# Performance work log

Hardware: AMD Instinct MI355X
Metric: run time of the kernel (lower is better)

Reference implementation:

```python
import jax, jax.numpy as jnp
import numpy as np

HIDDEN_DIM = 4096
NUM_EXPERTS = 64
THRESHOLD = 0.8


def setup_inputs() -> dict:
    key = jax.random.key(0)
    kx, kw = jax.random.split(key)
    x = jax.random.normal(kx, (4, 4096, HIDDEN_DIM), dtype=jnp.float32)
    # gate weight init: normal(0, 0.1), bias zeros (as in nn.init calls)
    W = jax.random.normal(kw, (HIDDEN_DIM, NUM_EXPERTS), dtype=jnp.float32) * 0.1
    b = jnp.zeros((NUM_EXPERTS,), dtype=jnp.float32)
    return {"x": x, "W": W, "b": b}


def reference(x, W, b):
    # logits: [B, S, E]
    logits = jnp.einsum('bsh,he->bse', x, W) + b
    probs = jax.nn.softmax(logits, axis=-1)
    # descending sort over experts
    order = jnp.argsort(-probs, axis=-1)                        # [B,S,E] int
    sorted_probs = jnp.take_along_axis(probs, order, axis=-1)   # [B,S,E]
    cum = jnp.cumsum(sorted_probs, axis=-1)
    mask = cum >= THRESHOLD                                     # [B,S,E] bool
    k_values = jnp.argmax(mask.astype(jnp.float32), axis=-1) + 1
    never = ~jnp.any(mask, axis=-1)
    k_values = jnp.where(never, NUM_EXPERTS, k_values)          # [B,S] int
    # Vectorized mask-and-scatter replacing the per-token Python loop.
    # Padded to NUM_EXPERTS (static max_k) for jit compatibility; slots
    # beyond k get expert=-1, prob=0 exactly as the torch fill defaults.
    slot = jnp.arange(NUM_EXPERTS)                              # [E]
    sel = slot[None, None, :] < k_values[..., None]             # [B,S,E]
    selected_experts = jnp.where(sel, order, -1)
    selected_probs = jnp.where(sel, sorted_probs, 0.0)
    return selected_experts, selected_probs, k_values
```

## Files before the change

kernel.cpp:

```cpp
#include <hip/hip_runtime.h>
#include <math.h>

#define HID 4096
#define NEXP 64
#define NTOK 16384
#define NCH 16

typedef __attribute__((ext_vector_type(8))) short short8;
typedef __attribute__((ext_vector_type(8))) __bf16 bf16x8;
typedef __attribute__((ext_vector_type(4))) float f32x4;

__global__ __launch_bounds__(256) void wfrag_kernel(
    const float* __restrict__ W, short* __restrict__ wfh,
    short* __restrict__ wfl, unsigned int* __restrict__ flag_count) {
  if (blockIdx.x == 0 && threadIdx.x == 0) *flag_count = 0u;
  int gid = blockIdx.x * 256 + threadIdx.x;
  int l  = gid & 63;
  int nt = (gid >> 6) & 3;
  int ks = gid >> 8;
  int e  = nt * 16 + (l & 15);
  int k0 = ks * 32 + (l >> 4) * 8;
  bf16x8 h8, l8;
#pragma unroll
  for (int j = 0; j < 8; ++j) {
    float w = W[(size_t)(k0 + j) * NEXP + e];
    __bf16 h = (__bf16)w;
    h8[j] = h;
    l8[j] = (__bf16)(w - (float)h);
  }
  ((short8*)wfh)[gid] = __builtin_bit_cast(short8, h8);
  ((short8*)wfl)[gid] = __builtin_bit_cast(short8, l8);
}

template <int P>
__device__ __forceinline__ void issue_b(const short8*& wh, const short8*& wl,
                                        short8 (&rbh)[2][8],
                                        short8 (&rbl)[2][8]) {
#pragma unroll
  for (int kk = 0; kk < 2; ++kk)
#pragma unroll
    for (int nt = 0; nt < 4; ++nt) {
      rbh[P][kk * 4 + nt] = wh[kk * 256 + nt * 64];
      rbl[P][kk * 4 + nt] = wl[kk * 256 + nt * 64];
    }
  wh += 512;
  wl += 512;
}

template <int P>
__device__ __forceinline__ void issue_g(const float* (&xp)[4][2],
                                        float* stage ) {
#pragma unroll
  for (int st = 0; st < 4; ++st)
#pragma unroll
    for (int n = 0; n < 4; ++n)
      __builtin_amdgcn_global_load_lds(xp[st][n & 1] + (n >> 1) * (8 * HID),
                                       stage + st * 1024 + n * 256, 16, 0, 0);
#pragma unroll
  for (int st = 0; st < 4; ++st) {
    xp[st][0] += 64;
    xp[st][1] += 64;
  }
}

template <int P>
__device__ __forceinline__ void compute_c(const float* stage,
                                          short8 (&rbh)[2][8],
                                          short8 (&rbl)[2][8],
                                          f32x4 (&acc)[4][4], int l) {
  const int lr = l >> 4;
  const char* cb = (const char*)stage;
#pragma unroll
  for (int kk = 0; kk < 2; ++kk) {
    int s0 = ((kk * 8 + lr * 2) ^ (l & 7)) * 16;
#pragma unroll
    for (int st = 0; st < 4; ++st) {
      const char* rowbase = cb + st * 4096 + (l & 15) * 256;
      float4 lo = *(const float4*)(rowbase + s0);
      float4 hi = *(const float4*)(rowbase + (s0 ^ 16));
      float xv[8] = {lo.x, lo.y, lo.z, lo.w, hi.x, hi.y, hi.z, hi.w};
      bf16x8 ah, al;
#pragma unroll
      for (int j = 0; j < 8; ++j) {
        __bf16 h = (__bf16)xv[j];
        ah[j] = h;
        al[j] = (__bf16)(xv[j] - (float)h);
      }
#pragma unroll
      for (int nt = 0; nt < 4; ++nt) {
        bf16x8 vh = __builtin_bit_cast(bf16x8, rbh[P][kk * 4 + nt]);
        bf16x8 vl = __builtin_bit_cast(bf16x8, rbl[P][kk * 4 + nt]);
        acc[st][nt] = __builtin_amdgcn_mfma_f32_16x16x32_bf16(ah, vh, acc[st][nt], 0, 0, 0);
        acc[st][nt] = __builtin_amdgcn_mfma_f32_16x16x32_bf16(al, vh, acc[st][nt], 0, 0, 0);
        acc[st][nt] = __builtin_amdgcn_mfma_f32_16x16x32_bf16(ah, vl, acc[st][nt], 0, 0, 0);
        acc[st][nt] = __builtin_amdgcn_mfma_f32_16x16x32_bf16(al, vl, acc[st][nt], 0, 0, 0);
      }
    }
  }
}

#define SB __builtin_amdgcn_sched_barrier(0)
#define WAIT32 asm volatile("s_waitcnt vmcnt(32)" ::: "memory")
#define WAIT0  asm volatile("s_waitcnt vmcnt(0)" ::: "memory")

__global__ __launch_bounds__(256) void gemm_kernel(
    const float* __restrict__ x, const short* __restrict__ wfh,
    const short* __restrict__ wfl, float* __restrict__ partial) {
  __shared__ float xstage[4][2][4096];

  const int t = threadIdx.x;
  const int q = t >> 6;
  const int l = t & 63;
  const int lr = l >> 4;
  const int m0 = blockIdx.x * 64;
  const int kq = q * (HID / 4);

  const float* xp[4][2];
#pragma unroll
  for (int st = 0; st < 4; ++st)
#pragma unroll
    for (int p = 0; p < 2; ++p) {
      int g = (l & 15) ^ (lr + 4 * p);
      int row = m0 + st * 16 + 4 * p + lr;
      xp[st][p] = x + (size_t)row * HID + kq + g * 4;
    }

  const short8* wh = (const short8*)wfh + (size_t)(q * 32) * 256 + l;
  const short8* wl = (const short8*)wfl + (size_t)(q * 32) * 256 + l;

  f32x4 acc[4][4];
#pragma unroll
  for (int st = 0; st < 4; ++st)
#pragma unroll
    for (int nt = 0; nt < 4; ++nt) acc[st][nt] = (f32x4){0.f, 0.f, 0.f, 0.f};

  short8 rbh[2][8], rbl[2][8];

  issue_b<0>(wh, wl, rbh, rbl);
  SB;
  issue_g<0>(xp, &xstage[q][0][0]);
  SB;

#pragma unroll 1
  for (int c2 = 0; c2 < 7; ++c2) {
    issue_b<1>(wh, wl, rbh, rbl);
    SB;
    issue_g<1>(xp, &xstage[q][1][0]);
    SB;
    WAIT32;
    SB;
    compute_c<0>(&xstage[q][0][0], rbh, rbl, acc, l);

    issue_b<0>(wh, wl, rbh, rbl);
    SB;
    issue_g<0>(xp, &xstage[q][0][0]);
    SB;
    WAIT32;
    SB;
    compute_c<1>(&xstage[q][1][0], rbh, rbl, acc, l);
  }
  issue_b<1>(wh, wl, rbh, rbl);
  SB;
  issue_g<1>(xp, &xstage[q][1][0]);
  SB;
  WAIT32;
  SB;
  compute_c<0>(&xstage[q][0][0], rbh, rbl, acc, l);
  WAIT0;
  SB;
  compute_c<1>(&xstage[q][1][0], rbh, rbl, acc, l);

#pragma unroll
  for (int st = 0; st < 4; ++st)
#pragma unroll
    for (int nt = 0; nt < 4; ++nt)
#pragma unroll
      for (int r = 0; r < 4; ++r)
        partial[((size_t)q * NTOK + m0 + st * 16 + lr * 4 + r) * NEXP +
                nt * 16 + (l & 15)] = acc[st][nt][r];
}

__global__ __launch_bounds__(256) void route_kernel(
    const float* __restrict__ partial, const float* __restrict__ b,
    float* __restrict__ out_exp, float* __restrict__ out_prob,
    float* __restrict__ out_k, unsigned int* __restrict__ flag_count,
    int* __restrict__ flag_list) {
  const int tok = (int)((blockIdx.x * 256 + threadIdx.x) >> 6);
  const int l   = threadIdx.x & 63;

  float p0 = partial[((size_t)0 * NTOK + tok) * NEXP + l];
  float p1 = partial[((size_t)1 * NTOK + tok) * NEXP + l];
  float p2 = partial[((size_t)2 * NTOK + tok) * NEXP + l];
  float p3 = partial[((size_t)3 * NTOK + tok) * NEXP + l];
  float lgv = (p0 + p1) + (p2 + p3) + b[l];

  float mx = lgv;
#pragma unroll
  for (int off = 32; off; off >>= 1) mx = fmaxf(mx, __shfl_xor(mx, off));
  float ev = expf(lgv - mx);
  float sm = ev;
#pragma unroll
  for (int off = 32; off; off >>= 1) sm += __shfl_xor(sm, off);
  float p = ev / sm;

  float sp = p;
  int   si = l;
#pragma unroll
  for (int k = 2; k <= 64; k <<= 1) {
#pragma unroll
    for (int j = k >> 1; j > 0; j >>= 1) {
      float op = __shfl_xor(sp, j);
      int   oi = __shfl_xor(si, j);
      bool cmp  = (sp > op) || (sp == op && si < oi);
      bool keep = (cmp == (((l & k) == 0) == ((l & j) == 0)));
      if (!keep) { sp = op; si = oi; }
    }
  }

  float c = sp;
#pragma unroll
  for (int off = 1; off < 64; off <<= 1) {
    float tp = __shfl_up(c, off);
    if (l >= off) c += tp;
  }

  unsigned long long m = __ballot(c >= 0.8f);
  int kv = (m == 0ULL) ? NEXP : __ffsll(m);

  float spn = __shfl_down(sp, 1);
  bool pairRisk = (l < kv) && (l < 63) && ((sp - spn) < 1e-3f * (sp + spn));
  bool cumRisk  = fabsf(c - 0.8f) < 3e-4f;
  bool flagged  = (__ballot(pairRisk || cumRisk) != 0ULL);

  bool sel = l < kv;
  size_t base = (size_t)tok * NEXP;
  out_exp[base + l]  = sel ? (float)si : -1.0f;
  out_prob[base + l] = sel ? sp : 0.0f;
  if (l == 0) {
    out_k[tok] = (float)kv;
    if (flagged) {
      unsigned int idx = atomicAdd(flag_count, 1u);
      flag_list[idx] = tok;
    }
  }
}

__global__ __launch_bounds__(256) void router_repair(
    const float* __restrict__ x, const float* __restrict__ W,
    const float* __restrict__ b, const unsigned int* __restrict__ flag_count,
    const int* __restrict__ flag_list, float* __restrict__ out_exp,
    float* __restrict__ out_prob, float* __restrict__ out_k) {
  __shared__ double part[4][NEXP];
  const int t = threadIdx.x;
  const int e = t & 63;
  const int c = t >> 6;
  const int n = (int)*flag_count;

  for (int i = blockIdx.x; i < n; i += gridDim.x) {
    const int tok = flag_list[i];
    const float* xrow = x + (size_t)tok * HID;
    double s = 0.0;
    const int k0 = c * (HID / 4);
#pragma unroll 8
    for (int k = k0; k < k0 + HID / 4; ++k)
      s = fma((double)xrow[k], (double)W[(size_t)k * NEXP + e], s);
    part[c][e] = s;
    __syncthreads();

    if (t < 64) {
      double lgv = ((part[0][e] + part[1][e]) + part[2][e]) + part[3][e] +
                   (double)b[e];
      double mx = lgv;
#pragma unroll
      for (int off = 32; off; off >>= 1) mx = fmax(mx, __shfl_xor(mx, off));
      double ev = exp(lgv - mx);
      double sm = ev;
#pragma unroll
      for (int off = 32; off; off >>= 1) sm += __shfl_xor(sm, off);
      double p = ev / sm;

      double sp = p;
      int    si = e;
#pragma unroll
      for (int k = 2; k <= 64; k <<= 1) {
#pragma unroll
        for (int j = k >> 1; j > 0; j >>= 1) {
          double op = __shfl_xor(sp, j);
          int    oi = __shfl_xor(si, j);
          bool cmp  = (sp > op) || (sp == op && si < oi);
          bool keep = (cmp == (((e & k) == 0) == ((e & j) == 0)));
          if (!keep) { sp = op; si = oi; }
        }
      }

      double cc = sp;
#pragma unroll
      for (int off = 1; off < 64; off <<= 1) {
        double tp = __shfl_up(cc, off);
        if (e >= off) cc += tp;
      }

      unsigned long long m = __ballot(cc >= 0.8);
      int kv = (m == 0ULL) ? NEXP : __ffsll(m);

      bool sel = e < kv;
      size_t base = (size_t)tok * NEXP;
      out_exp[base + e]  = sel ? (float)si : -1.0f;
      out_prob[base + e] = sel ? (float)sp : 0.0f;
      if (e == 0) out_k[tok] = (float)kv;
    }
    __syncthreads();
  }
}

extern "C" void kernel_launch(void* const* d_in, const int* in_sizes, int n_in,
                              void* d_out, int out_size, void* d_ws,
                              size_t ws_size, hipStream_t stream) {
  const float* x = (const float*)d_in[0];
  const float* W = (const float*)d_in[1];
  const float* b = (const float*)d_in[2];

  float* out_exp  = (float*)d_out;
  float* out_prob = out_exp + (size_t)NTOK * NEXP;
  float* out_k    = out_prob + (size_t)NTOK * NEXP;

  short* wfh = (short*)d_ws;
  short* wfl = (short*)((char*)d_ws + (size_t)512 * 1024);
  unsigned int* flag_count = (unsigned int*)((char*)d_ws + (size_t)1024 * 1024);
  int* flag_list = (int*)((char*)d_ws + (size_t)1024 * 1024 + 256);
  float* partial = (float*)((char*)d_ws + (size_t)2 * 1024 * 1024);

  wfrag_kernel<<<128, 256, 0, stream>>>(W, wfh, wfl, flag_count);
  gemm_kernel<<<NTOK / 64, 256, 0, stream>>>(x, wfh, wfl, partial);
  route_kernel<<<NTOK * NEXP / 256, 256, 0, stream>>>(
      partial, b, out_exp, out_prob, out_k, flag_count, flag_list);
  router_repair<<<128, 256, 0, stream>>>(x, W, b, flag_count, flag_list,
                                         out_exp, out_prob, out_k);
}
```

Baseline: 125.3 us.

## Fuse routing epilogue into GEMM kernel via shared-memory partial reduction

The routing softmax, sort, cumulative threshold and output writes are folded into the GEMM kernel. The four per-wave K-split partial accumulators go to padded shared memory (reusing the x staging buffer) instead of a global partial buffer. Each wave then reduces them and routes 16 tokens. This removes a kernel launch and the global write and re-read of the partial logits. In exchange the GEMM blocks run a serial per-token routing tail that may not overlap well with other blocks' memory traffic.

```diff
diff --git a/kernel.cpp b/kernel.cpp
--- a/kernel.cpp
+++ b/kernel.cpp
@@ -4,7 +4,7 @@
 #define HID 4096
 #define NEXP 64
 #define NTOK 16384
-#define NCH 16
+#define PSTRIDE 68
 
 typedef __attribute__((ext_vector_type(8))) short short8;
 typedef __attribute__((ext_vector_type(8))) __bf16 bf16x8;
@@ -103,10 +103,13 @@
 #define WAIT32 asm volatile("s_waitcnt vmcnt(32)" ::: "memory")
 #define WAIT0  asm volatile("s_waitcnt vmcnt(0)" ::: "memory")
 
-__global__ __launch_bounds__(256) void gemm_kernel(
+__global__ __launch_bounds__(256) void gemm_route_kernel(
     const float* __restrict__ x, const short* __restrict__ wfh,
-    const short* __restrict__ wfl, float* __restrict__ partial) {
-  __shared__ float xstage[4][2][4096];
+    const short* __restrict__ wfl, const float* __restrict__ b,
+    float* __restrict__ out_exp, float* __restrict__ out_prob,
+    float* __restrict__ out_k, unsigned int* __restrict__ flag_count,
+    int* __restrict__ flag_list) {
+  __shared__ float smem[32768];
 
   const int t = threadIdx.x;
   const int q = t >> 6;
@@ -115,6 +118,9 @@
   const int m0 = blockIdx.x * 64;
   const int kq = q * (HID / 4);
 
+  float* stage0 = smem + q * 8192;
+  float* stage1 = smem + q * 8192 + 4096;
+
   const float* xp[4][2];
 #pragma unroll
   for (int st = 0; st < 4; ++st)
@@ -138,109 +144,108 @@
 
   issue_b<0>(wh, wl, rbh, rbl);
   SB;
-  issue_g<0>(xp, &xstage[q][0][0]);
+  issue_g<0>(xp, stage0);
   SB;
 
 #pragma unroll 1
   for (int c2 = 0; c2 < 7; ++c2) {
     issue_b<1>(wh, wl, rbh, rbl);
     SB;
-    issue_g<1>(xp, &xstage[q][1][0]);
+    issue_g<1>(xp, stage1);
     SB;
     WAIT32;
     SB;
-    compute_c<0>(&xstage[q][0][0], rbh, rbl, acc, l);
+    compute_c<0>(stage0, rbh, rbl, acc, l);
 
     issue_b<0>(wh, wl, rbh, rbl);
     SB;
-    issue_g<0>(xp, &xstage[q][0][0]);
+    issue_g<0>(xp, stage0);
     SB;
     WAIT32;
     SB;
-    compute_c<1>(&xstage[q][1][0], rbh, rbl, acc, l);
+    compute_c<1>(stage1, rbh, rbl, acc, l);
   }
   issue_b<1>(wh, wl, rbh, rbl);
   SB;
-  issue_g<1>(xp, &xstage[q][1][0]);
+  issue_g<1>(xp, stage1);
   SB;
   WAIT32;
   SB;
-  compute_c<0>(&xstage[q][0][0], rbh, rbl, acc, l);
+  compute_c<0>(stage0, rbh, rbl, acc, l);
   WAIT0;
   SB;
-  compute_c<1>(&xstage[q][1][0], rbh, rbl, acc, l);
-
+  compute_c<1>(stage1, rbh, rbl, acc, l);
+
+  __syncthreads();
+  float* part = smem;
 #pragma unroll
   for (int st = 0; st < 4; ++st)
 #pragma unroll
     for (int nt = 0; nt < 4; ++nt)
 #pragma unroll
       for (int r = 0; r < 4; ++r)
-        partial[((size_t)q * NTOK + m0 + st * 16 + lr * 4 + r) * NEXP +
-                nt * 16 + (l & 15)] = acc[st][nt][r];
-}
-
-__global__ __launch_bounds__(256) void route_kernel(
-    const float* __restrict__ partial, const float* __restrict__ b,
-    float* __restrict__ out_exp, float* __restrict__ out_prob,
-    float* __restrict__ out_k, unsigned int* __restrict__ flag_count,
-    int* __restrict__ flag_list) {
-  const int tok = (int)((blockIdx.x * 256 + threadIdx.x) >> 6);
-  const int l   = threadIdx.x & 63;
-
-  float p0 = partial[((size_t)0 * NTOK + tok) * NEXP + l];
-  float p1 = partial[((size_t)1 * NTOK + tok) * NEXP + l];
-  float p2 = partial[((size_t)2 * NTOK + tok) * NEXP + l];
-  float p3 = partial[((size_t)3 * NTOK + tok) * NEXP + l];
-  float lgv = (p0 + p1) + (p2 + p3) + b[l];
-
-  float mx = lgv;
-#pragma unroll
-  for (int off = 32; off; off >>= 1) mx = fmaxf(mx, __shfl_xor(mx, off));
-  float ev = expf(lgv - mx);
-  float sm = ev;
-#pragma unroll
-  for (int off = 32; off; off >>= 1) sm += __shfl_xor(sm, off);
-  float p = ev / sm;
-
-  float sp = p;
-  int   si = l;
-#pragma unroll
-  for (int k = 2; k <= 64; k <<= 1) {
-#pragma unroll
-    for (int j = k >> 1; j > 0; j >>= 1) {
-      float op = __shfl_xor(sp, j);
-      int   oi = __shfl_xor(si, j);
-      bool cmp  = (sp > op) || (sp == op && si < oi);
-      bool keep = (cmp == (((l & k) == 0) == ((l & j) == 0)));
-      if (!keep) { sp = op; si = oi; }
-    }
-  }
-
-  float c = sp;
-#pragma unroll
-  for (int off = 1; off < 64; off <<= 1) {
-    float tp = __shfl_up(c, off);
-    if (l >= off) c += tp;
-  }
-
-  unsigned long long m = __ballot(c >= 0.8f);
-  int kv = (m == 0ULL) ? NEXP : __ffsll(m);
-
-  float spn = __shfl_down(sp, 1);
-  bool pairRisk = (l < kv) && (l < 63) && ((sp - spn) < 1e-3f * (sp + spn));
-  bool cumRisk  = fabsf(c - 0.8f) < 3e-4f;
-  bool flagged  = (__ballot(pairRisk || cumRisk) != 0ULL);
-
-  bool sel = l < kv;
-  size_t base = (size_t)tok * NEXP;
-  out_exp[base + l]  = sel ? (float)si : -1.0f;
-  out_prob[base + l] = sel ? sp : 0.0f;
-  if (l == 0) {
-    out_k[tok] = (float)kv;
-    if (flagged) {
-      unsigned int idx = atomicAdd(flag_count, 1u);
-      flag_list[idx] = tok;
+        part[(q * 64 + st * 16 + lr * 4 + r) * PSTRIDE + nt * 16 + (l & 15)] =
+            acc[st][nt][r];
+  __syncthreads();
+
+  const float bias = b[l];
+  for (int it = 0; it < 16; ++it) {
+    const int tl = q * 16 + it;
+    float lgv = (part[(0 * 64 + tl) * PSTRIDE + l] +
+                 part[(1 * 64 + tl) * PSTRIDE + l]) +
+                (part[(2 * 64 + tl) * PSTRIDE + l] +
+                 part[(3 * 64 + tl) * PSTRIDE + l]) +
+                bias;
+
+    float mx = lgv;
+#pragma unroll
+    for (int off = 32; off; off >>= 1) mx = fmaxf(mx, __shfl_xor(mx, off));
+    float ev = expf(lgv - mx);
+    float sm = ev;
+#pragma unroll
+    for (int off = 32; off; off >>= 1) sm += __shfl_xor(sm, off);
+    float p = ev / sm;
+
+    float sp = p;
+    int   si = l;
+#pragma unroll
+    for (int k = 2; k <= 64; k <<= 1) {
+#pragma unroll
+      for (int j = k >> 1; j > 0; j >>= 1) {
+        float op = __shfl_xor(sp, j);
+        int   oi = __shfl_xor(si, j);
+        bool cmp  = (sp > op) || (sp == op && si < oi);
+        bool keep = (cmp == (((l & k) == 0) == ((l & j) == 0)));
+        if (!keep) { sp = op; si = oi; }
+      }
+    }
+
+    float c = sp;
+#pragma unroll
+    for (int off = 1; off < 64; off <<= 1) {
+      float tp = __shfl_up(c, off);
+      if (l >= off) c += tp;
+    }
+
+    unsigned long long m = __ballot(c >= 0.8f);
+    int kv = (m == 0ULL) ? NEXP : __ffsll(m);
+
+    float spn = __shfl_down(sp, 1);
+    bool pairRisk = (l < kv) && (l < 63) && ((sp - spn) < 1e-3f * (sp + spn));
+    bool cumRisk  = fabsf(c - 0.8f) < 3e-4f;
+    bool flagged  = (__ballot(pairRisk || cumRisk) != 0ULL);
+
+    bool sel = l < kv;
+    const int tok = m0 + tl;
+    size_t base = (size_t)tok * NEXP;
+    out_exp[base + l]  = sel ? (float)si : -1.0f;
+    out_prob[base + l] = sel ? sp : 0.0f;
+    if (l == 0) {
+      out_k[tok] = (float)kv;
+      if (flagged) {
+        unsigned int idx = atomicAdd(flag_count, 1u);
+        flag_list[idx] = tok;
+      }
     }
   }
 }
@@ -328,12 +333,10 @@
   short* wfl = (short*)((char*)d_ws + (size_t)512 * 1024);
   unsigned int* flag_count = (unsigned int*)((char*)d_ws + (size_t)1024 * 1024);
   int* flag_list = (int*)((char*)d_ws + (size_t)1024 * 1024 + 256);
-  float* partial = (float*)((char*)d_ws + (size_t)2 * 1024 * 1024);
 
   wfrag_kernel<<<128, 256, 0, stream>>>(W, wfh, wfl, flag_count);
-  gemm_kernel<<<NTOK / 64, 256, 0, stream>>>(x, wfh, wfl, partial);
-  route_kernel<<<NTOK * NEXP / 256, 256, 0, stream>>>(
-      partial, b, out_exp, out_prob, out_k, flag_count, flag_list);
+  gemm_route_kernel<<<NTOK / 64, 256, 0, stream>>>(
+      x, wfh, wfl, b, out_exp, out_prob, out_k, flag_count, flag_list);
   router_repair<<<128, 256, 0, stream>>>(x, W, b, flag_count, flag_list,
                                          out_exp, out_prob, out_k);
 }
```

New measurement: 135.0 us. 7.7% more time.

## Split GEMM K across eight waves per block with in-LDS pairwise reduction

Applied to the files above, without the earlier changes.

The block grows from 256 to 512 threads, so each of the eight waves handles one eighth of the hidden dimension instead of one quarter. Each wave now moves half as much data per stage, and the LDS staging layout and swizzle are reworked to match. Waves 4-7 write their accumulators to shared memory, and waves 0-3 add them in before writing the same four partial slices as before. This raises wave-level parallelism and memory-level parallelism per block, at the cost of an extra LDS reduction, two block barriers, and possibly lower occupancy from the larger block.

```diff
diff --git a/kernel.cpp b/kernel.cpp
--- a/kernel.cpp
+++ b/kernel.cpp
@@ -4,7 +4,6 @@
 #define HID 4096
 #define NEXP 64
 #define NTOK 16384
-#define NCH 16
 
 typedef __attribute__((ext_vector_type(8))) short short8;
 typedef __attribute__((ext_vector_type(8))) __bf16 bf16x8;
@@ -34,99 +33,98 @@
 
 template <int P>
 __device__ __forceinline__ void issue_b(const short8*& wh, const short8*& wl,
-                                        short8 (&rbh)[2][8],
-                                        short8 (&rbl)[2][8]) {
-#pragma unroll
-  for (int kk = 0; kk < 2; ++kk)
-#pragma unroll
-    for (int nt = 0; nt < 4; ++nt) {
-      rbh[P][kk * 4 + nt] = wh[kk * 256 + nt * 64];
-      rbl[P][kk * 4 + nt] = wl[kk * 256 + nt * 64];
-    }
-  wh += 512;
-  wl += 512;
+                                        short8 (&rbh)[2][4],
+                                        short8 (&rbl)[2][4]) {
+#pragma unroll
+  for (int nt = 0; nt < 4; ++nt) {
+    rbh[P][nt] = wh[nt * 64];
+    rbl[P][nt] = wl[nt * 64];
+  }
+  wh += 256;
+  wl += 256;
 }
 
 template <int P>
 __device__ __forceinline__ void issue_g(const float* (&xp)[4][2],
-                                        float* stage ) {
+                                        float* wavebase ) {
 #pragma unroll
   for (int st = 0; st < 4; ++st)
 #pragma unroll
-    for (int n = 0; n < 4; ++n)
-      __builtin_amdgcn_global_load_lds(xp[st][n & 1] + (n >> 1) * (8 * HID),
-                                       stage + st * 1024 + n * 256, 16, 0, 0);
+    for (int p = 0; p < 2; ++p)
+      __builtin_amdgcn_global_load_lds(xp[st][p],
+                                       wavebase + P * 2048 + st * 512 + p * 256,
+                                       16, 0, 0);
 #pragma unroll
   for (int st = 0; st < 4; ++st) {
-    xp[st][0] += 64;
-    xp[st][1] += 64;
+    xp[st][0] += 32;
+    xp[st][1] += 32;
   }
 }
 
 template <int P>
-__device__ __forceinline__ void compute_c(const float* stage,
-                                          short8 (&rbh)[2][8],
-                                          short8 (&rbl)[2][8],
+__device__ __forceinline__ void compute_c(const float* wavebase,
+                                          short8 (&rbh)[2][4],
+                                          short8 (&rbl)[2][4],
                                           f32x4 (&acc)[4][4], int l) {
   const int lr = l >> 4;
-  const char* cb = (const char*)stage;
-#pragma unroll
-  for (int kk = 0; kk < 2; ++kk) {
-    int s0 = ((kk * 8 + lr * 2) ^ (l & 7)) * 16;
-#pragma unroll
-    for (int st = 0; st < 4; ++st) {
-      const char* rowbase = cb + st * 4096 + (l & 15) * 256;
-      float4 lo = *(const float4*)(rowbase + s0);
-      float4 hi = *(const float4*)(rowbase + (s0 ^ 16));
-      float xv[8] = {lo.x, lo.y, lo.z, lo.w, hi.x, hi.y, hi.z, hi.w};
-      bf16x8 ah, al;
-#pragma unroll
-      for (int j = 0; j < 8; ++j) {
-        __bf16 h = (__bf16)xv[j];
-        ah[j] = h;
-        al[j] = (__bf16)(xv[j] - (float)h);
-      }
-#pragma unroll
-      for (int nt = 0; nt < 4; ++nt) {
-        bf16x8 vh = __builtin_bit_cast(bf16x8, rbh[P][kk * 4 + nt]);
-        bf16x8 vl = __builtin_bit_cast(bf16x8, rbl[P][kk * 4 + nt]);
-        acc[st][nt] = __builtin_amdgcn_mfma_f32_16x16x32_bf16(ah, vh, acc[st][nt], 0, 0, 0);
-        acc[st][nt] = __builtin_amdgcn_mfma_f32_16x16x32_bf16(al, vh, acc[st][nt], 0, 0, 0);
-        acc[st][nt] = __builtin_amdgcn_mfma_f32_16x16x32_bf16(ah, vl, acc[st][nt], 0, 0, 0);
-        acc[st][nt] = __builtin_amdgcn_mfma_f32_16x16x32_bf16(al, vl, acc[st][nt], 0, 0, 0);
-      }
+  const int s0 = ((2 * lr) ^ (l & 7)) * 16;
+  const char* cb = (const char*)(wavebase + P * 2048);
+#pragma unroll
+  for (int st = 0; st < 4; ++st) {
+    const char* rowbase =
+        cb + st * 2048 + ((l >> 3) & 1) * 1024 + (l & 7) * 128;
+    float4 lo = *(const float4*)(rowbase + s0);
+    float4 hi = *(const float4*)(rowbase + (s0 ^ 16));
+    float xv[8] = {lo.x, lo.y, lo.z, lo.w, hi.x, hi.y, hi.z, hi.w};
+    bf16x8 ah, al;
+#pragma unroll
+    for (int j = 0; j < 8; ++j) {
+      __bf16 h = (__bf16)xv[j];
+      ah[j] = h;
+      al[j] = (__bf16)(xv[j] - (float)h);
+    }
+#pragma unroll
+    for (int nt = 0; nt < 4; ++nt) {
+      bf16x8 vh = __builtin_bit_cast(bf16x8, rbh[P][nt]);
+      bf16x8 vl = __builtin_bit_cast(bf16x8, rbl[P][nt]);
+      acc[st][nt] = __builtin_amdgcn_mfma_f32_16x16x32_bf16(ah, vh, acc[st][nt], 0, 0, 0);
+      acc[st][nt] = __builtin_amdgcn_mfma_f32_16x16x32_bf16(al, vh, acc[st][nt], 0, 0, 0);
+      acc[st][nt] = __builtin_amdgcn_mfma_f32_16x16x32_bf16(ah, vl, acc[st][nt], 0, 0, 0);
+      acc[st][nt] = __builtin_amdgcn_mfma_f32_16x16x32_bf16(al, vl, acc[st][nt], 0, 0, 0);
     }
   }
 }
 
 #define SB __builtin_amdgcn_sched_barrier(0)
-#define WAIT32 asm volatile("s_waitcnt vmcnt(32)" ::: "memory")
+#define WAIT16 asm volatile("s_waitcnt vmcnt(16)" ::: "memory")
 #define WAIT0  asm volatile("s_waitcnt vmcnt(0)" ::: "memory")
 
-__global__ __launch_bounds__(256) void gemm_kernel(
+__global__ __launch_bounds__(512, 2) void gemm_kernel(
     const float* __restrict__ x, const short* __restrict__ wfh,
     const short* __restrict__ wfl, float* __restrict__ partial) {
-  __shared__ float xstage[4][2][4096];
+  __shared__ float smem[32768];
 
   const int t = threadIdx.x;
-  const int q = t >> 6;
+  const int w = t >> 6;
   const int l = t & 63;
   const int lr = l >> 4;
   const int m0 = blockIdx.x * 64;
-  const int kq = q * (HID / 4);
+  const int kq = w * (HID / 8);
+
+  float* wavebase = smem + w * 4096;
 
   const float* xp[4][2];
 #pragma unroll
   for (int st = 0; st < 4; ++st)
 #pragma unroll
     for (int p = 0; p < 2; ++p) {
-      int g = (l & 15) ^ (lr + 4 * p);
-      int row = m0 + st * 16 + 4 * p + lr;
+      int g = (l & 7) ^ (l >> 3);
+      int row = m0 + st * 16 + 8 * p + (l >> 3);
       xp[st][p] = x + (size_t)row * HID + kq + g * 4;
     }
 
-  const short8* wh = (const short8*)wfh + (size_t)(q * 32) * 256 + l;
-  const short8* wl = (const short8*)wfl + (size_t)(q * 32) * 256 + l;
+  const short8* wh = (const short8*)wfh + (size_t)(w * 16 * 4) * 64 + l;
+  const short8* wl = (const short8*)wfl + (size_t)(w * 16 * 4) * 64 + l;
 
   f32x4 acc[4][4];
 #pragma unroll
@@ -134,50 +132,69 @@
 #pragma unroll
     for (int nt = 0; nt < 4; ++nt) acc[st][nt] = (f32x4){0.f, 0.f, 0.f, 0.f};
 
-  short8 rbh[2][8], rbl[2][8];
+  short8 rbh[2][4], rbl[2][4];
 
   issue_b<0>(wh, wl, rbh, rbl);
   SB;
-  issue_g<0>(xp, &xstage[q][0][0]);
+  issue_g<0>(xp, wavebase);
   SB;
 
 #pragma unroll 1
   for (int c2 = 0; c2 < 7; ++c2) {
     issue_b<1>(wh, wl, rbh, rbl);
     SB;
-    issue_g<1>(xp, &xstage[q][1][0]);
-    SB;
-    WAIT32;
-    SB;
-    compute_c<0>(&xstage[q][0][0], rbh, rbl, acc, l);
+    issue_g<1>(xp, wavebase);
+    SB;
+    WAIT16;
+    SB;
+    compute_c<0>(wavebase, rbh, rbl, acc, l);
 
     issue_b<0>(wh, wl, rbh, rbl);
     SB;
-    issue_g<0>(xp, &xstage[q][0][0]);
-    SB;
-    WAIT32;
-    SB;
-    compute_c<1>(&xstage[q][1][0], rbh, rbl, acc, l);
+    issue_g<0>(xp, wavebase);
+    SB;
+    WAIT16;
+    SB;
+    compute_c<1>(wavebase, rbh, rbl, acc, l);
   }
   issue_b<1>(wh, wl, rbh, rbl);
   SB;
-  issue_g<1>(xp, &xstage[q][1][0]);
-  SB;
-  WAIT32;
-  SB;
-  compute_c<0>(&xstage[q][0][0], rbh, rbl, acc, l);
+  issue_g<1>(xp, wavebase);
+  SB;
+  WAIT16;
+  SB;
+  compute_c<0>(wavebase, rbh, rbl, acc, l);
   WAIT0;
   SB;
-  compute_c<1>(&xstage[q][1][0], rbh, rbl, acc, l);
-
-#pragma unroll
-  for (int st = 0; st < 4; ++st)
-#pragma unroll
-    for (int nt = 0; nt < 4; ++nt)
-#pragma unroll
-      for (int r = 0; r < 4; ++r)
-        partial[((size_t)q * NTOK + m0 + st * 16 + lr * 4 + r) * NEXP +
-                nt * 16 + (l & 15)] = acc[st][nt][r];
+  compute_c<1>(wavebase, rbh, rbl, acc, l);
+
+  __syncthreads();
+  float* red = smem;
+  if (w >= 4) {
+#pragma unroll
+    for (int st = 0; st < 4; ++st)
+#pragma unroll
+      for (int nt = 0; nt < 4; ++nt)
+#pragma unroll
+        for (int r = 0; r < 4; ++r)
+          red[((w - 4) * 64 + st * 16 + lr * 4 + r) * 68 + nt * 16 +
+              (l & 15)] = acc[st][nt][r];
+  }
+  __syncthreads();
+  if (w < 4) {
+#pragma unroll
+    for (int st = 0; st < 4; ++st)
+#pragma unroll
+      for (int nt = 0; nt < 4; ++nt)
+#pragma unroll
+        for (int r = 0; r < 4; ++r) {
+          int row = st * 16 + lr * 4 + r;
+          float s = acc[st][nt][r] +
+                    red[(w * 64 + row) * 68 + nt * 16 + (l & 15)];
+          partial[((size_t)w * NTOK + m0 + row) * NEXP + nt * 16 + (l & 15)] =
+              s;
+        }
+  }
 }
 
 __global__ __launch_bounds__(256) void route_kernel(
@@ -331,7 +348,7 @@
   float* partial = (float*)((char*)d_ws + (size_t)2 * 1024 * 1024);
 
   wfrag_kernel<<<128, 256, 0, stream>>>(W, wfh, wfl, flag_count);
-  gemm_kernel<<<NTOK / 64, 256, 0, stream>>>(x, wfh, wfl, partial);
+  gemm_kernel<<<NTOK / 64, 512, 0, stream>>>(x, wfh, wfl, partial);
   route_kernel<<<NTOK * NEXP / 256, 256, 0, stream>>>(
       partial, b, out_exp, out_prob, out_k, flag_count, flag_list);
   router_repair<<<128, 256, 0, stream>>>(x, W, b, flag_count, flag_list,
```

Result: faster. 117.4 us (-6.3%).
